# Optimization experiments

Measured on AMD Instinct MI355X. Metric: run time of the kernel, lower is better.

## Reference

```python
import jax, jax.numpy as jnp
import numpy as np

EPS = 1e-8
VOX_WIDTH = 1.0
CURV_THRESH = 0.5


def _build_kernels():
    """Nine 3x3x3 central finite-difference stencils, pre-divided by vox_width / vox_width^2."""
    def zk():
        return np.zeros((3, 3, 3), np.float32)
    ks = {}
    # first derivatives (central difference), denominator vox_width
    for name, ax in (('ddx', 0), ('ddy', 1), ('ddz', 2)):
        k = zk(); i = [1, 1, 1]
        i[ax] = 0; k[tuple(i)] = -0.5
        i[ax] = 2; k[tuple(i)] = 0.5
        ks[name] = k / VOX_WIDTH
    # pure second derivatives, denominator vox_width^2
    for name, ax in (('d2dx2', 0), ('d2dy2', 1), ('d2dz2', 2)):
        k = zk(); i = [1, 1, 1]
        i[ax] = 0; k[tuple(i)] = 1.0
        i[ax] = 1; k[tuple(i)] = -2.0
        i[ax] = 2; k[tuple(i)] = 1.0
        ks[name] = k / VOX_WIDTH ** 2
    # mixed second derivatives, denominator vox_width^2
    for name, (a, b) in (('d2dxdy', (0, 1)), ('d2dxdz', (0, 2)), ('d2dydz', (1, 2))):
        k = zk()
        for sa, sb, v in ((0, 0, 0.25), (0, 2, -0.25), (2, 0, -0.25), (2, 2, 0.25)):
            i = [1, 1, 1]; i[a] = sa; i[b] = sb; k[tuple(i)] = v
        ks[name] = k / VOX_WIDTH ** 2
    order = ['ddx', 'ddy', 'ddz', 'd2dx2', 'd2dy2', 'd2dz2', 'd2dxdy', 'd2dxdz', 'd2dydz']
    return np.stack([ks[n] for n in order])[:, None]  # [9, 1, 3, 3, 3]


_KERNELS = jnp.asarray(_build_kernels())


def setup_inputs() -> dict:
    key = jax.random.key(0)
    phi = jax.random.normal(key, (2, 1, 192, 192, 192), dtype=jnp.float32)
    return {"phi": phi}


def reference(phi):
    # all nine stencils as one valid 3D conv: [N, 9, D-2, H-2, W-2]
    g = jax.lax.conv_general_dilated(
        phi, _KERNELS, window_strides=(1, 1, 1), padding='VALID',
        dimension_numbers=('NCDHW', 'OIDHW', 'NCDHW'))
    gx, gy, gz, hxx, hyy, hzz, hxy, hxz, hyz = (g[:, i:i + 1] for i in range(9))

    mag = jnp.sqrt(gx * gx + gy * gy + gz * gz + EPS)
    mag3 = mag ** 3

    # mean curvature: sum_{i!=j} g_i^2 H_jj - 2 sum_{i<j} g_i g_j H_ij, over |grad|^3
    cross = gx * gy * hxy + gx * gz * hxz + gy * gz * hyz
    mean_c = (gx * gx * (hyy + hzz) + gy * gy * (hxx + hzz) + gz * gz * (hxx + hyy)
              - 2.0 * cross) / (mag3 + EPS)

    # gaussian curvature: laplacian/|grad| - (g^T H g)/|grad|^3
    lap = (hxx + hyy + hzz) / (mag + EPS)
    quad = (gx * gx * hxx + gy * gy * hyy + gz * gz * hzz + 2.0 * cross) / (mag3 + EPS)
    gauss = lap - quad

    k1 = mean_c + jnp.sqrt(jnp.abs(mean_c ** 2 - gauss) + EPS)
    pen = jax.nn.relu((k1 / (CURV_THRESH + EPS)) ** 2 - 1.0)

    # zero crossings of phi over 3x3x3 neighborhoods (valid -> matches conv output shape)
    mn = jax.lax.reduce_window(phi, jnp.inf, jax.lax.min, (1, 1, 3, 3, 3), (1, 1, 1, 1, 1), 'VALID')
    mx = jax.lax.reduce_window(phi, -jnp.inf, jax.lax.max, (1, 1, 3, 3, 3), (1, 1, 1, 1, 1), 'VALID')
    phi_zero = jax.lax.stop_gradient((mn * mx < 0).astype(phi.dtype))

    return jnp.sum(phi_zero * pen) / (jnp.sum(phi_zero) + EPS)
```

## Files before the change

### kernel.cpp

```cpp
#include <hip/hip_runtime.h>


typedef float v2f __attribute__((ext_vector_type(2)));

constexpr int DIM  = 192;
constexpr int ODIM = 190;
constexpr int TX = 32, TY = 32, CZ = 19;
constexpr int NTX = 6, NTY = 6, NTZ = 10;
constexpr int PLANE = DIM * DIM;
constexpr int NBLOCKS = 2 * NTZ * NTY * NTX;

struct Slice {
    v2f   q[3][4];
    float xmn[4], xmx[4];
};

__global__ __launch_bounds__(256, 3) void curv_main(const float* __restrict__ phi,
                                                    double* __restrict__ acc,
                                                    int use_partials) {
    int bx = blockIdx.x;
    const int tx = bx % NTX; bx /= NTX;
    const int ty = bx % NTY; bx /= NTY;
    const int tz = bx % NTZ; bx /= NTZ;
    const int n  = bx;

    const int xbase = tx * TX, ybase = ty * TY, zbase = tz * CZ;
    const int tid = threadIdx.x;
    const int row = tid >> 3;
    const int x0  = (tid & 7) * 4;
    const float* pn = phi + (long long)n * DIM * PLANE;

    const int c4 = xbase + x0;
    int c2t = c4 + 4; if (c2t > DIM - 2) c2t = DIM - 2;
    const int c2 = c2t;
    int yoff[3];
#pragma unroll
    for (int dy = 0; dy < 3; ++dy) {
        int iy = ybase + row + dy; if (iy > DIM - 1) iy = DIM - 1;
        yoff[dy] = iy * DIM;
    }

    float4 t4[3]; float2 t2[3];
    auto pref_at = [&](const float* base) {
#pragma unroll
        for (int dy = 0; dy < 3; ++dy) {
            t4[dy] = *(const float4*)(base + yoff[dy] + c4);
            t2[dy] = *(const float2*)(base + yoff[dy] + c2);
        }
    };

    auto unpack = [&](Slice& s) {
        float mn6[6], mx6[6];
#pragma unroll
        for (int dy = 0; dy < 3; ++dy) {
            const float4 a = t4[dy]; const float2 b = t2[dy];
            s.q[dy][0] = (v2f){a.x, a.z};
            s.q[dy][1] = (v2f){a.y, a.w};
            s.q[dy][2] = (v2f){a.z, b.x};
            s.q[dy][3] = (v2f){a.w, b.y};
            if (dy == 0) {
                mn6[0] = a.x; mn6[1] = a.y; mn6[2] = a.z;
                mn6[3] = a.w; mn6[4] = b.x; mn6[5] = b.y;
                mx6[0] = a.x; mx6[1] = a.y; mx6[2] = a.z;
                mx6[3] = a.w; mx6[4] = b.x; mx6[5] = b.y;
            } else {
                mn6[0] = fminf(mn6[0], a.x); mx6[0] = fmaxf(mx6[0], a.x);
                mn6[1] = fminf(mn6[1], a.y); mx6[1] = fmaxf(mx6[1], a.y);
                mn6[2] = fminf(mn6[2], a.z); mx6[2] = fmaxf(mx6[2], a.z);
                mn6[3] = fminf(mn6[3], a.w); mx6[3] = fmaxf(mx6[3], a.w);
                mn6[4] = fminf(mn6[4], b.x); mx6[4] = fmaxf(mx6[4], b.x);
                mn6[5] = fminf(mn6[5], b.y); mx6[5] = fmaxf(mx6[5], b.y);
            }
        }
#pragma unroll
        for (int j = 0; j < 4; ++j) {
            s.xmn[j] = fminf(fminf(mn6[j], mn6[j + 1]), mn6[j + 2]);
            s.xmx[j] = fmaxf(fmaxf(mx6[j], mx6[j + 1]), mx6[j + 2]);
        }
    };

    float fsp = 0.0f, fsc = 0.0f;
    const float EPSF = 1e-8f;
    const float EPS4 = 4e-8f;
    const int oy = ybase + row;

    bool vmask[4];
#pragma unroll
    for (int j = 0; j < 4; ++j)
        vmask[j] = (oy < ODIM) && (xbase + x0 + j < ODIM);

    auto compute = [&](const Slice& s0, const Slice& s1, const Slice& s2) {
        float wmn[4], wmx[4];
#pragma unroll
        for (int j = 0; j < 4; ++j) {
            wmn[j] = fminf(fminf(s0.xmn[j], s1.xmn[j]), s2.xmn[j]);
            wmx[j] = fmaxf(fmaxf(s0.xmx[j], s1.xmx[j]), s2.xmx[j]);
        }

#pragma unroll
        for (int p = 0; p < 2; ++p) {
            v2f Gx = s2.q[1][p + 1] - s0.q[1][p + 1];
            v2f Gy = s1.q[2][p + 1] - s1.q[0][p + 1];
            v2f Gz = s1.q[1][p + 2] - s1.q[1][p];

            v2f c2v = 2.0f * s1.q[1][p + 1];
            v2f hxx = s0.q[1][p + 1] - c2v + s2.q[1][p + 1];
            v2f hyy = s1.q[0][p + 1] - c2v + s1.q[2][p + 1];
            v2f hzz = s1.q[1][p] - c2v + s1.q[1][p + 2];

            v2f Mxy = s0.q[0][p + 1] - s0.q[2][p + 1]
                    - s2.q[0][p + 1] + s2.q[2][p + 1];
            v2f Mxz = s0.q[1][p] - s0.q[1][p + 2]
                    - s2.q[1][p] + s2.q[1][p + 2];
            v2f Myz = s1.q[0][p] - s1.q[0][p + 2]
                    - s1.q[2][p] + s1.q[2][p + 2];

            v2f Gx2 = Gx * Gx, Gy2 = Gy * Gy, Gz2 = Gz * Gz;
            v2f mag2G = Gx2 + Gy2 + Gz2 + EPS4;

            v2f r = (v2f){ __builtin_amdgcn_rsqf(mag2G.x),
                           __builtin_amdgcn_rsqf(mag2G.y) };
            v2f r3 = r * r * r;
            v2f twor3 = r3 + r3;

            v2f crossG = Gx * Gy * Mxy + Gx * Gz * Mxz + Gy * Gz * Myz;

            v2f num1 = Gx2 * (hyy + hzz) + Gy2 * (hxx + hzz) +
                       Gz2 * (hxx + hyy) - 0.5f * crossG;
            v2f mean_c = num1 * twor3;
            v2f lap   = (hxx + hyy + hzz) * (r + r);
            v2f num2  = Gx2 * hxx + Gy2 * hyy + Gz2 * hzz + 0.5f * crossG;
            v2f quad  = num2 * twor3;
            v2f gauss = lap - quad;

            v2f disc = mean_c * mean_c - gauss;
            v2f sq = (v2f){ sqrtf(fabsf(disc.x) + EPSF),
                            sqrtf(fabsf(disc.y) + EPSF) };
            v2f k1 = mean_c + sq;
            v2f t  = 2.0f * k1;
            v2f pen2 = t * t - 1.0f;

#pragma unroll
            for (int e = 0; e < 2; ++e) {
                const int j = p + 2 * e;
                float pen = fmaxf(e ? pen2.y : pen2.x, 0.0f);
                if (vmask[j] && (wmn[j] * wmx[j] < 0.0f)) {
                    fsp += pen;
                    fsc += 1.0f;
                }
            }
        }
    };

    Slice s0, s1, s2;

    const float* pz = pn + zbase * PLANE;
    pref_at(pz); pz += PLANE;  unpack(s0);
    pref_at(pz); pz += PLANE;  unpack(s1);
    pref_at(pz); pz += PLANE;

#pragma unroll 1
    for (int k = 0; k < 6; ++k) {
        unpack(s2); pref_at(pz); pz += PLANE; compute(s0, s1, s2);
        unpack(s0); pref_at(pz); pz += PLANE; compute(s1, s2, s0);
        unpack(s1); pref_at(pz); pz += PLANE; compute(s2, s0, s1);
    }
    unpack(s2);                           compute(s0, s1, s2);

    double sp = (double)fsp, sc = (double)fsc;
#pragma unroll
    for (int off = 32; off > 0; off >>= 1) {
        sp += __shfl_down(sp, off, 64);
        sc += __shfl_down(sc, off, 64);
    }

    __shared__ double lsp[4], lsc[4];
    const int wave = tid >> 6, lane = tid & 63;
    if (lane == 0) { lsp[wave] = sp; lsc[wave] = sc; }
    __syncthreads();
    if (tid == 0) {
        double tp = lsp[0] + lsp[1] + lsp[2] + lsp[3];
        double tc = lsc[0] + lsc[1] + lsc[2] + lsc[3];
        if (use_partials) {
            acc[2 * blockIdx.x]     = tp;
            acc[2 * blockIdx.x + 1] = tc;
        } else {
            atomicAdd(&acc[0], tp);
            atomicAdd(&acc[1], tc);
        }
    }
}

__global__ __launch_bounds__(256) void curv_reduce(const double* __restrict__ part,
                                                   int nblocks, int use_partials,
                                                   float* __restrict__ out) {
    double sp = 0.0, sc = 0.0;
    if (use_partials) {
        for (int i = threadIdx.x; i < nblocks; i += 256) {
            sp += part[2 * i];
            sc += part[2 * i + 1];
        }
    } else if (threadIdx.x == 0) {
        sp = part[0]; sc = part[1];
    }
#pragma unroll
    for (int off = 32; off > 0; off >>= 1) {
        sp += __shfl_down(sp, off, 64);
        sc += __shfl_down(sc, off, 64);
    }
    __shared__ double lsp[4], lsc[4];
    const int wave = threadIdx.x >> 6, lane = threadIdx.x & 63;
    if (lane == 0) { lsp[wave] = sp; lsc[wave] = sc; }
    __syncthreads();
    if (threadIdx.x == 0) {
        double tp = lsp[0] + lsp[1] + lsp[2] + lsp[3];
        double tc = lsc[0] + lsc[1] + lsc[2] + lsc[3];
        out[0] = (float)(tp / (tc + 1e-8));
    }
}

extern "C" void kernel_launch(void* const* d_in, const int* in_sizes, int n_in,
                              void* d_out, int out_size, void* d_ws, size_t ws_size,
                              hipStream_t stream) {
    const float* phi = (const float*)d_in[0];
    float* out = (float*)d_out;
    double* acc = (double*)d_ws;

    const int use_partials = (ws_size >= (size_t)(2 * NBLOCKS) * sizeof(double)) ? 1 : 0;
    if (!use_partials) {
        hipMemsetAsync(d_ws, 0, 2 * sizeof(double), stream);
    }

    curv_main<<<NBLOCKS, 256, 0, stream>>>(phi, acc, use_partials);
    curv_reduce<<<1, 256, 0, stream>>>(acc, NBLOCKS, use_partials, out);
}
```

Before: 108.5 us.

## Stage z-planes into LDS via async global_load_lds with 4-deep ring buffer

Replaces per-thread redundant global loads of each z-plane (three overlapping rows per thread) with cooperative async global-to-LDS DMA of each 34x40 plane tile into a 4-slot ring buffer. Threads then read their stencil rows from LDS, and vmcnt waits plus barriers pipeline loads several planes ahead. This cuts redundant global and L2 traffic and hides load latency. In exchange it adds a barrier per plane and about 22KB of LDS per block, which may reduce occupancy. The slice loop is also fully unrolled.

Result: slower. 112.3 us (+3.5%).

```diff
diff --git a/kernel.cpp b/kernel.cpp
--- a/kernel.cpp
+++ b/kernel.cpp
@@ -10,14 +10,28 @@
 constexpr int PLANE = DIM * DIM;
 constexpr int NBLOCKS = 2 * NTZ * NTY * NTX;
 
+constexpr int LROW   = 40;
+constexpr int LPLANE = 34 * LROW;
+
 struct Slice {
     v2f   q[3][4];
     float xmn[4], xmx[4];
 };
 
+#define GLDS(srcp, dstp)                                                   \
+    __builtin_amdgcn_global_load_lds(                                      \
+        (const __attribute__((address_space(1))) void*)(srcp),             \
+        (__attribute__((address_space(3))) void*)(dstp), 16, 0, 0)
+
+#define WVM(n)  asm volatile("s_waitcnt vmcnt(" #n ")" ::: "memory")
+#define BAR()   do { __builtin_amdgcn_s_barrier();                         \
+                     asm volatile("" ::: "memory"); } while (0)
+
 __global__ __launch_bounds__(256, 3) void curv_main(const float* __restrict__ phi,
                                                     double* __restrict__ acc,
                                                     int use_partials) {
+    __shared__ float lds[4 * LPLANE];
+
     int bx = blockIdx.x;
     const int tx = bx % NTX; bx /= NTX;
     const int ty = bx % NTY; bx /= NTY;
@@ -28,56 +42,62 @@
     const int tid = threadIdx.x;
     const int row = tid >> 3;
     const int x0  = (tid & 7) * 4;
-    const float* pn = phi + (long long)n * DIM * PLANE;
-
-    const int c4 = xbase + x0;
-    int c2t = c4 + 4; if (c2t > DIM - 2) c2t = DIM - 2;
-    const int c2 = c2t;
-    int yoff[3];
-#pragma unroll
-    for (int dy = 0; dy < 3; ++dy) {
-        int iy = ybase + row + dy; if (iy > DIM - 1) iy = DIM - 1;
-        yoff[dy] = iy * DIM;
-    }
-
-    float4 t4[3]; float2 t2[3];
-    auto pref_at = [&](const float* base) {
-#pragma unroll
-        for (int dy = 0; dy < 3; ++dy) {
-            t4[dy] = *(const float4*)(base + yoff[dy] + c4);
-            t2[dy] = *(const float2*)(base + yoff[dy] + c2);
-        }
-    };
-
-    auto unpack = [&](Slice& s) {
-        float mn6[6], mx6[6];
-#pragma unroll
-        for (int dy = 0; dy < 3; ++dy) {
-            const float4 a = t4[dy]; const float2 b = t2[dy];
-            s.q[dy][0] = (v2f){a.x, a.z};
-            s.q[dy][1] = (v2f){a.y, a.w};
-            s.q[dy][2] = (v2f){a.z, b.x};
-            s.q[dy][3] = (v2f){a.w, b.y};
-            if (dy == 0) {
-                mn6[0] = a.x; mn6[1] = a.y; mn6[2] = a.z;
-                mn6[3] = a.w; mn6[4] = b.x; mn6[5] = b.y;
-                mx6[0] = a.x; mx6[1] = a.y; mx6[2] = a.z;
-                mx6[3] = a.w; mx6[4] = b.x; mx6[5] = b.y;
-            } else {
-                mn6[0] = fminf(mn6[0], a.x); mx6[0] = fmaxf(mx6[0], a.x);
-                mn6[1] = fminf(mn6[1], a.y); mx6[1] = fmaxf(mx6[1], a.y);
-                mn6[2] = fminf(mn6[2], a.z); mx6[2] = fmaxf(mx6[2], a.z);
-                mn6[3] = fminf(mn6[3], a.w); mx6[3] = fmaxf(mx6[3], a.w);
-                mn6[4] = fminf(mn6[4], b.x); mx6[4] = fmaxf(mx6[4], b.x);
-                mn6[5] = fminf(mn6[5], b.y); mx6[5] = fmaxf(mx6[5], b.y);
-            }
-        }
-#pragma unroll
-        for (int j = 0; j < 4; ++j) {
-            s.xmn[j] = fminf(fminf(mn6[j], mn6[j + 1]), mn6[j + 2]);
-            s.xmx[j] = fmaxf(fmaxf(mx6[j], mx6[j + 1]), mx6[j + 2]);
-        }
-    };
+    const float* pn  = phi + (long long)n * DIM * PLANE;
+    const float* pzb = pn + (long long)zbase * PLANE;
+
+    const int lane = tid & 63, wave = tid >> 6;
+    const int chA = tid;
+    const int chB = 256 + wave * 21 + lane;
+    const bool bAct = lane < 21;
+    int rA = ybase + chA / 10;       if (rA > DIM - 1) rA = DIM - 1;
+    int cA = xbase + (chA % 10) * 4; if (cA > DIM - 4) cA = DIM - 4;
+    const int offA = rA * DIM + cA;
+    int rB = ybase + chB / 10;       if (rB > DIM - 1) rB = DIM - 1;
+    int cB = xbase + (chB % 10) * 4; if (cB > DIM - 4) cB = DIM - 4;
+    const int offB = rB * DIM + cB;
+
+#define STAGE(g, bi) do {                                                  \
+    const float* b_ = pzb + (g) * PLANE;                                   \
+    GLDS(b_ + offA, &lds[(bi) * LPLANE + chA * 4]);                        \
+    if (bAct) GLDS(b_ + offB, &lds[(bi) * LPLANE + chB * 4]);              \
+} while (0)
+
+    int lro[3];
+#pragma unroll
+    for (int dy = 0; dy < 3; ++dy) lro[dy] = (row + dy) * LROW;
+    int c2r = x0 + 4;
+    if (xbase + c2r > DIM - 2) c2r = DIM - 2 - xbase;
+
+#define UNPACKL(S, bi) do {                                                \
+    const float* lb_ = &lds[(bi) * LPLANE];                                \
+    float mn6[6], mx6[6];                                                  \
+    _Pragma("unroll")                                                      \
+    for (int dy = 0; dy < 3; ++dy) {                                       \
+        const float4 a = *(const float4*)(lb_ + lro[dy] + x0);             \
+        const float2 b = *(const float2*)(lb_ + lro[dy] + c2r);            \
+        (S).q[dy][0] = (v2f){a.x, a.z};                                    \
+        (S).q[dy][1] = (v2f){a.y, a.w};                                    \
+        (S).q[dy][2] = (v2f){a.z, b.x};                                    \
+        (S).q[dy][3] = (v2f){a.w, b.y};                                    \
+        if (dy == 0) {                                                     \
+            mn6[0] = a.x; mn6[1] = a.y; mn6[2] = a.z;                      \
+            mn6[3] = a.w; mn6[4] = b.x; mn6[5] = b.y;                      \
+            mx6[0] = a.x; mx6[1] = a.y; mx6[2] = a.z;                      \
+            mx6[3] = a.w; mx6[4] = b.x; mx6[5] = b.y;                      \
+        } else {                                                           \
+            mn6[0] = fminf(mn6[0], a.x); mx6[0] = fmaxf(mx6[0], a.x);      \
+            mn6[1] = fminf(mn6[1], a.y); mx6[1] = fmaxf(mx6[1], a.y);      \
+            mn6[2] = fminf(mn6[2], a.z); mx6[2] = fmaxf(mx6[2], a.z);      \
+            mn6[3] = fminf(mn6[3], a.w); mx6[3] = fmaxf(mx6[3], a.w);      \
+            mn6[4] = fminf(mn6[4], b.x); mx6[4] = fmaxf(mx6[4], b.x);      \
+            mn6[5] = fminf(mn6[5], b.y); mx6[5] = fmaxf(mx6[5], b.y);      \
+        }                                                                  \
+    }                                                                      \
+    _Pragma("unroll")                                                      \
+    for (int j = 0; j < 4; ++j) {                                          \
+        (S).xmn[j] = fminf(fminf(mn6[j], mn6[j + 1]), mn6[j + 2]);         \
+        (S).xmx[j] = fmaxf(fmaxf(mx6[j], mx6[j + 1]), mx6[j + 2]);         \
+    } } while (0)
 
     float fsp = 0.0f, fsc = 0.0f;
     const float EPSF = 1e-8f;
@@ -154,18 +174,34 @@
 
     Slice s0, s1, s2;
 
-    const float* pz = pn + zbase * PLANE;
-    pref_at(pz); pz += PLANE;  unpack(s0);
-    pref_at(pz); pz += PLANE;  unpack(s1);
-    pref_at(pz); pz += PLANE;
-
-#pragma unroll 1
-    for (int k = 0; k < 6; ++k) {
-        unpack(s2); pref_at(pz); pz += PLANE; compute(s0, s1, s2);
-        unpack(s0); pref_at(pz); pz += PLANE; compute(s1, s2, s0);
-        unpack(s1); pref_at(pz); pz += PLANE; compute(s2, s0, s1);
-    }
-    unpack(s2);                           compute(s0, s1, s2);
+    STAGE(0, 0); STAGE(1, 1); STAGE(2, 2); STAGE(3, 3);
+    WVM(6); BAR();
+    UNPACKL(s0, 0);
+    WVM(4); BAR();
+    STAGE(4, 0);
+    UNPACKL(s1, 1);
+    WVM(4); BAR();
+    STAGE(5, 1);
+
+    UNPACKL(s2, 2); compute(s0, s1, s2); WVM(4); BAR(); STAGE(6, 2);
+    UNPACKL(s0, 3); compute(s1, s2, s0); WVM(4); BAR(); STAGE(7, 3);
+    UNPACKL(s1, 0); compute(s2, s0, s1); WVM(4); BAR(); STAGE(8, 0);
+    UNPACKL(s2, 1); compute(s0, s1, s2); WVM(4); BAR(); STAGE(9, 1);
+    UNPACKL(s0, 2); compute(s1, s2, s0); WVM(4); BAR(); STAGE(10, 2);
+    UNPACKL(s1, 3); compute(s2, s0, s1); WVM(4); BAR(); STAGE(11, 3);
+    UNPACKL(s2, 0); compute(s0, s1, s2); WVM(4); BAR(); STAGE(12, 0);
+    UNPACKL(s0, 1); compute(s1, s2, s0); WVM(4); BAR(); STAGE(13, 1);
+    UNPACKL(s1, 2); compute(s2, s0, s1); WVM(4); BAR(); STAGE(14, 2);
+    UNPACKL(s2, 3); compute(s0, s1, s2); WVM(4); BAR(); STAGE(15, 3);
+    UNPACKL(s0, 0); compute(s1, s2, s0); WVM(4); BAR(); STAGE(16, 0);
+    UNPACKL(s1, 1); compute(s2, s0, s1); WVM(4); BAR(); STAGE(17, 1);
+    UNPACKL(s2, 2); compute(s0, s1, s2); WVM(4); BAR(); STAGE(18, 2);
+    UNPACKL(s0, 3); compute(s1, s2, s0); WVM(4); BAR(); STAGE(19, 3);
+    UNPACKL(s1, 0); compute(s2, s0, s1); WVM(4); BAR(); STAGE(20, 0);
+    UNPACKL(s2, 1); compute(s0, s1, s2); WVM(4); BAR();
+    UNPACKL(s0, 2); compute(s1, s2, s0); WVM(2); BAR();
+    UNPACKL(s1, 3); compute(s2, s0, s1); WVM(0); BAR();
+    UNPACKL(s2, 0); compute(s0, s1, s2);
 
     double sp = (double)fsp, sc = (double)fsc;
 #pragma unroll
@@ -175,7 +211,6 @@
     }
 
     __shared__ double lsp[4], lsc[4];
-    const int wave = tid >> 6, lane = tid & 63;
     if (lane == 0) { lsp[wave] = sp; lsc[wave] = sc; }
     __syncthreads();
     if (tid == 0) {
```
